# Kernel tuning notes

Hardware: AMD Instinct MI355X
Metric: run time of the kernel (lower is better)

The kernel has to match this reference:

```python
import jax, jax.numpy as jnp
import numpy as np

E = 8          # num_experts
TOP_K = 2
D = 1024       # hidden_size
I_MOE = 1024   # moe_intermediate_size (per-expert)
I_SH = 4096    # intermediate_size (shared expert)


def setup_inputs() -> dict:
    key = jax.random.key(0)
    ks = jax.random.split(key, 9)
    s = 0.02
    return {
        "hidden_states": jax.random.normal(ks[0], (2, 4096, D), dtype=jnp.float32),
        "gate_w": jax.random.normal(ks[1], (D, E), dtype=jnp.float32) * s,
        "eg": jax.random.normal(ks[2], (E, D, I_MOE), dtype=jnp.float32) * s,  # gate_proj per expert
        "eu": jax.random.normal(ks[3], (E, D, I_MOE), dtype=jnp.float32) * s,  # up_proj per expert
        "ed": jax.random.normal(ks[4], (E, I_MOE, D), dtype=jnp.float32) * s,  # down_proj per expert
        "sg": jax.random.normal(ks[5], (D, I_SH), dtype=jnp.float32) * s,
        "su": jax.random.normal(ks[6], (D, I_SH), dtype=jnp.float32) * s,
        "sd": jax.random.normal(ks[7], (I_SH, D), dtype=jnp.float32) * s,
        "shared_gate_w": jax.random.normal(ks[8], (D, 1), dtype=jnp.float32) * s,
    }


def _swiglu(x, wg, wu, wd):
    # down_proj(silu(gate_proj(x)) * up_proj(x))
    return (jax.nn.silu(x @ wg) * (x @ wu)) @ wd


def reference(hidden_states, gate_w, eg, eu, ed, sg, su, sd, shared_gate_w):
    B, S, Dm = hidden_states.shape
    x = hidden_states.reshape(-1, Dm)                     # [T, D]

    router_logits = x @ gate_w                            # [T, E]
    probs = jax.nn.softmax(router_logits.astype(jnp.float32), axis=-1)
    topw, topi = jax.lax.top_k(probs, TOP_K)              # [T, K]
    topw = topw / jnp.clip(jnp.sum(topw, axis=-1, keepdims=True), 1e-6)
    topw = topw.astype(x.dtype)

    # combine[t, e] = routing weight of expert e for token t (0 if unselected)
    combine = jnp.sum(jax.nn.one_hot(topi, E, dtype=x.dtype) * topw[..., None], axis=1)  # [T, E]

    out = jnp.zeros_like(x)
    for e in range(E):  # fixed small expert loop (structurally distinct weights)
        out = out + combine[:, e:e + 1] * _swiglu(x, eg[e], eu[e], ed[e])

    shared = _swiglu(x, sg, su, sd)
    shared_gate = jax.nn.sigmoid(x @ shared_gate_w)       # [T, 1]
    out = out + shared_gate * shared

    return out.reshape(B, S, Dm), router_logits
```

## Files before the change

### kernel.cpp

```cpp
#include <hip/hip_runtime.h>
#include <hip/hip_bf16.h>
#include <stdint.h>

#define T_TOK 8192
#define DDIM 1024
#define NEXP 8
#define IMOE 1024
#define ISH 4096
#define BK 64
#define PADTOT 17408

typedef __attribute__((ext_vector_type(8))) short short8;
typedef __attribute__((ext_vector_type(8))) __bf16 bf16x8;
typedef __attribute__((ext_vector_type(4))) float floatx4;

__device__ __forceinline__ unsigned short f2bf(float f) {
  union { float f; unsigned u; } v; v.f = f;
  unsigned r = v.u + 0x7fffu + ((v.u >> 16) & 1u);
  return (unsigned short)(r >> 16);
}

__device__ __forceinline__ floatx4 mfma16(short8 a, short8 b, floatx4 c) {
  return __builtin_amdgcn_mfma_f32_16x16x32_bf16(
      __builtin_bit_cast(bf16x8, a), __builtin_bit_cast(bf16x8, b), c, 0, 0, 0);
}

__device__ __forceinline__ void gload16(const void* g, void* l) {
  __builtin_amdgcn_global_load_lds((const __attribute__((address_space(1))) void*)g,
                                   (__attribute__((address_space(3))) void*)l, 16, 0, 0);
}



__global__ void k_cast(const float* __restrict__ src, unsigned short* __restrict__ dst, int n) {
  int i = (blockIdx.x * blockDim.x + threadIdx.x) * 4;
  if (i < n) {
    float4 v = *(const float4*)(src + i);
    ushort4 o;
    o.x = f2bf(v.x); o.y = f2bf(v.y); o.z = f2bf(v.z); o.w = f2bf(v.w);
    *(ushort4*)(dst + i) = o;
  }
}

__global__ void k_transpose_cast(const float* __restrict__ src, unsigned short* __restrict__ dst,
                                 int R, int C) {
  __shared__ float tile[32][33];
  int b = blockIdx.z;
  int c0 = blockIdx.x * 32, r0 = blockIdx.y * 32;
  const float* s = src + (size_t)b * R * C;
  unsigned short* d = dst + (size_t)b * R * C;
  int tx = threadIdx.x, ty = threadIdx.y;
#pragma unroll
  for (int j = 0; j < 32; j += 8)
    tile[ty + j][tx] = s[(size_t)(r0 + ty + j) * C + c0 + tx];
  __syncthreads();
#pragma unroll
  for (int j = 0; j < 32; j += 8)
    d[(size_t)(c0 + ty + j) * R + r0 + tx] = f2bf(tile[tx][ty + j]);
}


__global__ void k_router(const float* __restrict__ x, const float* __restrict__ gw,
                         const float* __restrict__ sgw, float* __restrict__ logits_out,
                         int* __restrict__ topi, float* __restrict__ topw,
                         float* __restrict__ sgate) {
  int wave = threadIdx.x >> 6;
  int lane = threadIdx.x & 63;
  int t = blockIdx.x * 4 + wave;
  const float* xr = x + (size_t)t * DDIM;
  float acc[9];
#pragma unroll
  for (int j = 0; j < 9; j++) acc[j] = 0.f;
  for (int d = lane; d < DDIM; d += 64) {
    float xv = xr[d];
    const float* g = gw + d * 8;
    float4 g0 = *(const float4*)g;
    float4 g1 = *(const float4*)(g + 4);
    acc[0] += xv * g0.x; acc[1] += xv * g0.y; acc[2] += xv * g0.z; acc[3] += xv * g0.w;
    acc[4] += xv * g1.x; acc[5] += xv * g1.y; acc[6] += xv * g1.z; acc[7] += xv * g1.w;
    acc[8] += xv * sgw[d];
  }
#pragma unroll
  for (int off = 32; off > 0; off >>= 1) {
#pragma unroll
    for (int j = 0; j < 9; j++) acc[j] += __shfl_xor(acc[j], off);
  }
  if (lane == 0) {
#pragma unroll
    for (int j = 0; j < 8; j++) logits_out[t * 8 + j] = acc[j];
    int i0 = 0;
#pragma unroll
    for (int j = 1; j < 8; j++) if (acc[j] > acc[i0]) i0 = j;
    int i1 = -1;
#pragma unroll
    for (int j = 0; j < 8; j++) {
      if (j == i0) continue;
      if (i1 < 0 || acc[j] > acc[i1]) i1 = j;
    }
    float e1 = expf(acc[i1] - acc[i0]);
    float inv = 1.f / (1.f + e1);
    topi[t * 2] = i0; topi[t * 2 + 1] = i1;
    topw[t * 2] = inv; topw[t * 2 + 1] = e1 * inv;
    sgate[t] = 1.f / (1.f + expf(-acc[8]));
  }
}

__global__ void k_hist(const int* __restrict__ topi, int* __restrict__ blockhist) {
  __shared__ int h[NEXP];
  if (threadIdx.x < NEXP) h[threadIdx.x] = 0;
  __syncthreads();
  int i = blockIdx.x * 256 + threadIdx.x;
  atomicAdd(&h[topi[i]], 1);
  __syncthreads();
  if (threadIdx.x < NEXP) blockhist[blockIdx.x * NEXP + threadIdx.x] = h[threadIdx.x];
}

__global__ void k_offsets(const int* __restrict__ blockhist, int* __restrict__ pseg,
                          int* __restrict__ rcnt, int* __restrict__ blockbase) {
  if (threadIdx.x == 0) {
    int tot[NEXP];
#pragma unroll
    for (int e = 0; e < NEXP; e++) tot[e] = 0;
    for (int b = 0; b < 64; b++)
      for (int e = 0; e < NEXP; e++) {
        blockbase[b * NEXP + e] = tot[e];
        tot[e] += blockhist[b * NEXP + e];
      }
    int s = 0;
    for (int e = 0; e < NEXP; e++) {
      rcnt[e] = tot[e];
      pseg[e] = s;
      s += (tot[e] + 127) & ~127;
    }
    pseg[NEXP] = s;
    for (int b = 0; b < 64; b++)
      for (int e = 0; e < NEXP; e++) blockbase[b * NEXP + e] += pseg[e];
  }
}

__global__ void k_scatter(const int* __restrict__ topi, const float* __restrict__ topw,
                          const int* __restrict__ blockbase,
                          int* __restrict__ ptok, float* __restrict__ pw) {
  __shared__ int cur[NEXP];
  if (threadIdx.x < NEXP) cur[threadIdx.x] = blockbase[blockIdx.x * NEXP + threadIdx.x];
  __syncthreads();
  int i = blockIdx.x * 256 + threadIdx.x;
  int e = topi[i];
  int pos = atomicAdd(&cur[e], 1);
  ptok[pos] = i >> 1;
  pw[pos] = topw[i];
}

__global__ void k_gather(const unsigned short* __restrict__ xb, const int* __restrict__ ptok,
                         unsigned short* __restrict__ xg) {
  int row = blockIdx.x * 2 + (threadIdx.x >> 7);
  int col = (threadIdx.x & 127) * 8;
  int tok = ptok[row];
  uint4 v = make_uint4(0, 0, 0, 0);
  if (tok >= 0 && tok < T_TOK) v = *(const uint4*)(xb + (size_t)tok * DDIM + col);
  *(uint4*)(xg + (size_t)row * DDIM + col) = v;
}

__global__ __launch_bounds__(256, 4) void k_gu_shared(
    const unsigned short* __restrict__ Xb,
    const unsigned short* __restrict__ BgT,
    const unsigned short* __restrict__ BuT,
    unsigned short* __restrict__ H)
{
  __shared__ __align__(16) unsigned short As[128 * BK];
  __shared__ __align__(16) unsigned short Bgs[64 * BK];
  __shared__ __align__(16) unsigned short Bus[64 * BK];

  const int tm0 = blockIdx.x * 128;
  const int tn0 = blockIdx.y * 64;
  const int tid = threadIdx.x;
  const int wave = tid >> 6, lane = tid & 63;
  const int wm = wave & 1, wn = wave >> 1;
  const int quad = lane >> 4, l16 = lane & 15;
  const int srow = lane >> 3;
  const int scol = ((lane & 7) ^ srow) * 8;

  floatx4 accg[4][2] = {};
  floatx4 accu[4][2] = {};

  for (int k0 = 0; k0 < DDIM; k0 += BK) {
#pragma unroll
    for (int s = 0; s < 4; s++) {
      int rb = (wave * 4 + s) * 8;
      gload16(Xb + (size_t)(tm0 + rb + srow) * DDIM + k0 + scol, As + rb * BK);
    }
#pragma unroll
    for (int s = 0; s < 2; s++) {
      int rb = (wave * 2 + s) * 8;
      gload16(BgT + (size_t)(tn0 + rb + srow) * DDIM + k0 + scol, Bgs + rb * BK);
      gload16(BuT + (size_t)(tn0 + rb + srow) * DDIM + k0 + scol, Bus + rb * BK);
    }
    __syncthreads();
#pragma unroll
    for (int ks = 0; ks < BK; ks += 32) {
      short8 af[4], bg[2], bu[2];
#pragma unroll
      for (int f = 0; f < 4; f++) {
        int r = wm * 64 + f * 16 + l16;
        af[f] = *(const short8*)(As + r * BK + ((((ks >> 3) + quad) ^ (r & 7)) << 3));
      }
#pragma unroll
      for (int f = 0; f < 2; f++) {
        int r = wn * 32 + f * 16 + l16;
        int off = r * BK + ((((ks >> 3) + quad) ^ (r & 7)) << 3);
        bg[f] = *(const short8*)(Bgs + off);
        bu[f] = *(const short8*)(Bus + off);
      }
#pragma unroll
      for (int fm = 0; fm < 4; fm++)
#pragma unroll
        for (int fn = 0; fn < 2; fn++) {
          accg[fm][fn] = mfma16(af[fm], bg[fn], accg[fm][fn]);
          accu[fm][fn] = mfma16(af[fm], bu[fn], accu[fm][fn]);
        }
    }
    __syncthreads();
  }
#pragma unroll
  for (int fm = 0; fm < 4; fm++)
#pragma unroll
    for (int reg = 0; reg < 4; reg++) {
      int r = tm0 + wm * 64 + fm * 16 + quad * 4 + reg;
#pragma unroll
      for (int fn = 0; fn < 2; fn++) {
        int c = tn0 + wn * 32 + fn * 16 + l16;
        float g = accg[fm][fn][reg];
        float u = accu[fm][fn][reg];
        float h = (g / (1.f + __expf(-g))) * u;
        H[(size_t)r * ISH + c] = f2bf(h);
      }
    }
}

__global__ __launch_bounds__(256, 4) void k_gu_expert(
    const unsigned short* __restrict__ Xg,
    const unsigned short* __restrict__ EgT,
    const unsigned short* __restrict__ EuT,
    const int* __restrict__ pseg,
    unsigned short* __restrict__ Hp)
{
  const int m0 = blockIdx.x * 128;
  if (m0 >= pseg[NEXP]) return;
  int e = 0;
#pragma unroll
  for (int j = 1; j < NEXP; j++) if (m0 >= pseg[j]) e = j;

  __shared__ __align__(16) unsigned short As[128 * BK];
  __shared__ __align__(16) unsigned short Bgs[64 * BK];
  __shared__ __align__(16) unsigned short Bus[64 * BK];

  const int tn0 = blockIdx.y * 64;
  const int tid = threadIdx.x;
  const int wave = tid >> 6, lane = tid & 63;
  const int wm = wave & 1, wn = wave >> 1;
  const int quad = lane >> 4, l16 = lane & 15;
  const int srow = lane >> 3;
  const int scol = ((lane & 7) ^ srow) * 8;

  const unsigned short* Bg = EgT + (size_t)e * IMOE * DDIM;
  const unsigned short* Bu = EuT + (size_t)e * IMOE * DDIM;

  floatx4 accg[4][2] = {};
  floatx4 accu[4][2] = {};

  for (int k0 = 0; k0 < DDIM; k0 += BK) {
#pragma unroll
    for (int s = 0; s < 4; s++) {
      int rb = (wave * 4 + s) * 8;
      gload16(Xg + (size_t)(m0 + rb + srow) * DDIM + k0 + scol, As + rb * BK);
    }
#pragma unroll
    for (int s = 0; s < 2; s++) {
      int rb = (wave * 2 + s) * 8;
      gload16(Bg + (size_t)(tn0 + rb + srow) * DDIM + k0 + scol, Bgs + rb * BK);
      gload16(Bu + (size_t)(tn0 + rb + srow) * DDIM + k0 + scol, Bus + rb * BK);
    }
    __syncthreads();
#pragma unroll
    for (int ks = 0; ks < BK; ks += 32) {
      short8 af[4], bg[2], bu[2];
#pragma unroll
      for (int f = 0; f < 4; f++) {
        int r = wm * 64 + f * 16 + l16;
        af[f] = *(const short8*)(As + r * BK + ((((ks >> 3) + quad) ^ (r & 7)) << 3));
      }
#pragma unroll
      for (int f = 0; f < 2; f++) {
        int r = wn * 32 + f * 16 + l16;
        int off = r * BK + ((((ks >> 3) + quad) ^ (r & 7)) << 3);
        bg[f] = *(const short8*)(Bgs + off);
        bu[f] = *(const short8*)(Bus + off);
      }
#pragma unroll
      for (int fm = 0; fm < 4; fm++)
#pragma unroll
        for (int fn = 0; fn < 2; fn++) {
          accg[fm][fn] = mfma16(af[fm], bg[fn], accg[fm][fn]);
          accu[fm][fn] = mfma16(af[fm], bu[fn], accu[fm][fn]);
        }
    }
    __syncthreads();
  }
#pragma unroll
  for (int fm = 0; fm < 4; fm++)
#pragma unroll
    for (int reg = 0; reg < 4; reg++) {
      int r = m0 + wm * 64 + fm * 16 + quad * 4 + reg;
#pragma unroll
      for (int fn = 0; fn < 2; fn++) {
        int c = tn0 + wn * 32 + fn * 16 + l16;
        float g = accg[fm][fn][reg];
        float u = accu[fm][fn][reg];
        Hp[(size_t)r * IMOE + c] = f2bf((g / (1.f + __expf(-g))) * u);
      }
    }
}

__global__ __launch_bounds__(256, 4) void k_down_shared(
    const unsigned short* __restrict__ Hsh,
    const unsigned short* __restrict__ SdT,
    const float* __restrict__ sgate,
    float* __restrict__ out)
{
  __shared__ __align__(16) unsigned short As[128 * BK];
  __shared__ __align__(16) unsigned short Bs[128 * BK];

  const int tm0 = blockIdx.x * 128;
  const int tn0 = blockIdx.y * 128;
  const int tid = threadIdx.x;
  const int wave = tid >> 6, lane = tid & 63;
  const int wm = wave & 1, wn = wave >> 1;
  const int quad = lane >> 4, l16 = lane & 15;
  const int srow = lane >> 3;
  const int scol = ((lane & 7) ^ srow) * 8;

  floatx4 acc[4][4] = {};

  for (int k0 = 0; k0 < ISH; k0 += BK) {
#pragma unroll
    for (int s = 0; s < 4; s++) {
      int rb = (wave * 4 + s) * 8;
      gload16(Hsh + (size_t)(tm0 + rb + srow) * ISH + k0 + scol, As + rb * BK);
      gload16(SdT + (size_t)(tn0 + rb + srow) * ISH + k0 + scol, Bs + rb * BK);
    }
    __syncthreads();
#pragma unroll
    for (int ks = 0; ks < BK; ks += 32) {
      short8 af[4], bfr[4];
#pragma unroll
      for (int f = 0; f < 4; f++) {
        int ra = wm * 64 + f * 16 + l16;
        int rb2 = wn * 64 + f * 16 + l16;
        af[f] = *(const short8*)(As + ra * BK + ((((ks >> 3) + quad) ^ (ra & 7)) << 3));
        bfr[f] = *(const short8*)(Bs + rb2 * BK + ((((ks >> 3) + quad) ^ (rb2 & 7)) << 3));
      }
#pragma unroll
      for (int fm = 0; fm < 4; fm++)
#pragma unroll
        for (int fn = 0; fn < 4; fn++)
          acc[fm][fn] = mfma16(af[fm], bfr[fn], acc[fm][fn]);
    }
    __syncthreads();
  }
#pragma unroll
  for (int fm = 0; fm < 4; fm++)
#pragma unroll
    for (int reg = 0; reg < 4; reg++) {
      int r = tm0 + wm * 64 + fm * 16 + quad * 4 + reg;
      float gt = sgate[r];
#pragma unroll
      for (int fn = 0; fn < 4; fn++) {
        int c = tn0 + wn * 64 + fn * 16 + l16;
        out[(size_t)r * DDIM + c] = gt * acc[fm][fn][reg];
      }
    }
}

__global__ __launch_bounds__(256, 4) void k_down_expert(
    const unsigned short* __restrict__ Hp,
    const unsigned short* __restrict__ EdT,
    const int* __restrict__ pseg,
    const int* __restrict__ rcnt,
    const int* __restrict__ ptok,
    const float* __restrict__ pw,
    float* __restrict__ out)
{
  const int m0 = blockIdx.x * 128;
  if (m0 >= pseg[NEXP]) return;
  int e = 0;
#pragma unroll
  for (int j = 1; j < NEXP; j++) if (m0 >= pseg[j]) e = j;
  const int sbase = pseg[e];
  const int cnt = rcnt[e];

  __shared__ __align__(16) unsigned short As[128 * BK];
  __shared__ __align__(16) unsigned short Bs[128 * BK];

  const int tn0 = blockIdx.y * 128;
  const int tid = threadIdx.x;
  const int wave = tid >> 6, lane = tid & 63;
  const int wm = wave & 1, wn = wave >> 1;
  const int quad = lane >> 4, l16 = lane & 15;
  const int srow = lane >> 3;
  const int scol = ((lane & 7) ^ srow) * 8;

  const unsigned short* B = EdT + (size_t)e * IMOE * DDIM;

  floatx4 acc[4][4] = {};

  for (int k0 = 0; k0 < IMOE; k0 += BK) {
#pragma unroll
    for (int s = 0; s < 4; s++) {
      int rb = (wave * 4 + s) * 8;
      gload16(Hp + (size_t)(m0 + rb + srow) * IMOE + k0 + scol, As + rb * BK);
      gload16(B + (size_t)(tn0 + rb + srow) * IMOE + k0 + scol, Bs + rb * BK);
    }
    __syncthreads();
#pragma unroll
    for (int ks = 0; ks < BK; ks += 32) {
      short8 af[4], bfr[4];
#pragma unroll
      for (int f = 0; f < 4; f++) {
        int ra = wm * 64 + f * 16 + l16;
        int rb2 = wn * 64 + f * 16 + l16;
        af[f] = *(const short8*)(As + ra * BK + ((((ks >> 3) + quad) ^ (ra & 7)) << 3));
        bfr[f] = *(const short8*)(Bs + rb2 * BK + ((((ks >> 3) + quad) ^ (rb2 & 7)) << 3));
      }
#pragma unroll
      for (int fm = 0; fm < 4; fm++)
#pragma unroll
        for (int fn = 0; fn < 4; fn++)
          acc[fm][fn] = mfma16(af[fm], bfr[fn], acc[fm][fn]);
    }
    __syncthreads();
  }
#pragma unroll
  for (int fm = 0; fm < 4; fm++)
#pragma unroll
    for (int reg = 0; reg < 4; reg++) {
      int grow = m0 + wm * 64 + fm * 16 + quad * 4 + reg;
      if (grow - sbase < cnt) {
        int t = ptok[grow];
        float w = pw[grow];
#pragma unroll
        for (int fn = 0; fn < 4; fn++) {
          int c = tn0 + wn * 64 + fn * 16 + l16;
          atomicAdd(&out[(size_t)t * DDIM + c], w * acc[fm][fn][reg]);
        }
      }
    }
}


extern "C" void kernel_launch(void* const* d_in, const int* in_sizes, int n_in,
                              void* d_out, int out_size, void* d_ws, size_t ws_size,
                              hipStream_t stream) {
  const float* x   = (const float*)d_in[0];
  const float* gw  = (const float*)d_in[1];
  const float* eg  = (const float*)d_in[2];
  const float* eu  = (const float*)d_in[3];
  const float* ed  = (const float*)d_in[4];
  const float* sg  = (const float*)d_in[5];
  const float* su  = (const float*)d_in[6];
  const float* sd  = (const float*)d_in[7];
  const float* sgw = (const float*)d_in[8];

  float* out    = (float*)d_out;
  float* logits = out + (size_t)T_TOK * DDIM;

  char* ws = (char*)d_ws;
  unsigned short* xb   = (unsigned short*)(ws + 0);
  unsigned short* egT  = (unsigned short*)(ws + 16777216);
  unsigned short* euT  = (unsigned short*)(ws + 33554432);
  unsigned short* edT  = (unsigned short*)(ws + 50331648);
  unsigned short* sgT  = (unsigned short*)(ws + 67108864);
  unsigned short* suT  = (unsigned short*)(ws + 75497472);
  unsigned short* sdT  = (unsigned short*)(ws + 83886080);
  unsigned short* hsh  = (unsigned short*)(ws + 92274688);
  unsigned short* xg   = (unsigned short*)(ws + 92274688);
  unsigned short* hp   = (unsigned short*)(ws + 159383552);
  int*   topi      = (int*)  (ws + 195035136);
  float* topw      = (float*)(ws + 195100672);
  float* sgate     = (float*)(ws + 195166208);
  int*   ptok      = (int*)  (ws + 195198976);
  float* pw        = (float*)(ws + 195268608);
  int*   blockhist = (int*)  (ws + 195338240);
  int*   blockbase = (int*)  (ws + 195340288);
  int*   pseg      = (int*)  (ws + 195342336);
  int*   rcnt      = (int*)  (ws + 195342400);

  k_cast<<<8192, 256, 0, stream>>>(x, xb, T_TOK * DDIM);
  k_transpose_cast<<<dim3(32, 32, 8), dim3(32, 8), 0, stream>>>(eg, egT, DDIM, IMOE);
  k_transpose_cast<<<dim3(32, 32, 8), dim3(32, 8), 0, stream>>>(eu, euT, DDIM, IMOE);
  k_transpose_cast<<<dim3(32, 32, 8), dim3(32, 8), 0, stream>>>(ed, edT, IMOE, DDIM);
  k_transpose_cast<<<dim3(128, 32, 1), dim3(32, 8), 0, stream>>>(sg, sgT, DDIM, ISH);
  k_transpose_cast<<<dim3(128, 32, 1), dim3(32, 8), 0, stream>>>(su, suT, DDIM, ISH);
  k_transpose_cast<<<dim3(32, 128, 1), dim3(32, 8), 0, stream>>>(sd, sdT, ISH, DDIM);

  k_router<<<T_TOK / 4, 256, 0, stream>>>(x, gw, sgw, logits, topi, topw, sgate);
  k_hist<<<64, 256, 0, stream>>>(topi, blockhist);
  k_offsets<<<1, 64, 0, stream>>>(blockhist, pseg, rcnt, blockbase);
  k_scatter<<<64, 256, 0, stream>>>(topi, topw, blockbase, ptok, pw);
  k_gather<<<PADTOT / 2, 256, 0, stream>>>(xb, ptok, xg);

  k_gu_expert<<<dim3(PADTOT / 128, 16), 256, 0, stream>>>(xg, egT, euT, pseg, hp);
  k_gu_shared<<<dim3(64, 64), 256, 0, stream>>>(xb, sgT, suT, hsh);
  k_down_shared<<<dim3(64, 8), 256, 0, stream>>>(hsh, sdT, sgate, out);
  k_down_expert<<<dim3(PADTOT / 128, 8), 256, 0, stream>>>(hp, edT, pseg, rcnt, ptok, pw, out);

  (void)in_sizes; (void)n_in; (void)out_size; (void)ws_size;
}
```

Before: 685.5 us.

## Replace gate/up GEMMs with 256x128 double-buffered 8-wave kernel with fused gather

Replaces the separate shared and expert gate/up GEMM kernels with one templated 512-thread kernel. It uses 256x128 tiles, double-buffered LDS, interleaved async loads with MFMA phases, and s_setprio scheduling hints. The expert path reads token rows straight from xb through ptok, which removes the separate gather kernel and its xg buffer. Expert segments are padded to 256 rows via a new vseg array. The cost is higher register and LDS pressure, and more wasted padding rows per expert.

Measured after the change: 680.4 us. No clear change (-0.8%).

```diff
diff --git a/kernel.cpp b/kernel.cpp
--- a/kernel.cpp
+++ b/kernel.cpp
@@ -116,7 +116,8 @@
 }
 
 __global__ void k_offsets(const int* __restrict__ blockhist, int* __restrict__ pseg,
-                          int* __restrict__ rcnt, int* __restrict__ blockbase) {
+                          int* __restrict__ rcnt, int* __restrict__ blockbase,
+                          int* __restrict__ vseg) {
   if (threadIdx.x == 0) {
     int tot[NEXP];
 #pragma unroll
@@ -126,13 +127,16 @@
         blockbase[b * NEXP + e] = tot[e];
         tot[e] += blockhist[b * NEXP + e];
       }
-    int s = 0;
+    int s = 0, vs = 0;
     for (int e = 0; e < NEXP; e++) {
       rcnt[e] = tot[e];
       pseg[e] = s;
+      vseg[e] = vs;
       s += (tot[e] + 127) & ~127;
+      vs += (tot[e] + 255) & ~255;
     }
     pseg[NEXP] = s;
+    vseg[NEXP] = vs;
     for (int b = 0; b < 64; b++)
       for (int e = 0; e < NEXP; e++) blockbase[b * NEXP + e] += pseg[e];
   }
@@ -151,175 +155,167 @@
   pw[pos] = topw[i];
 }
 
-__global__ void k_gather(const unsigned short* __restrict__ xb, const int* __restrict__ ptok,
-                         unsigned short* __restrict__ xg) {
-  int row = blockIdx.x * 2 + (threadIdx.x >> 7);
-  int col = (threadIdx.x & 127) * 8;
-  int tok = ptok[row];
-  uint4 v = make_uint4(0, 0, 0, 0);
-  if (tok >= 0 && tok < T_TOK) v = *(const uint4*)(xb + (size_t)tok * DDIM + col);
-  *(uint4*)(xg + (size_t)row * DDIM + col) = v;
-}
-
-__global__ __launch_bounds__(256, 4) void k_gu_shared(
-    const unsigned short* __restrict__ Xb,
-    const unsigned short* __restrict__ BgT,
-    const unsigned short* __restrict__ BuT,
+
+#define STG_A(NB, KK, P) gload16(ArowP[P] + (KK), &As[NB][((P)*64 + wave * 8) * BK])
+#define STG_G(NB, KK, P) gload16(Bgrow + (size_t)(P) * 64 * DDIM + (KK), &Bgs[NB][((P)*64 + wave * 8) * BK])
+#define STG_U(NB, KK, P) gload16(Burow + (size_t)(P) * 64 * DDIM + (KK), &Bus[NB][((P)*64 + wave * 8) * BK])
+
+#define GU_PHASE(CB, MGI, MGOFF, SW, G0, G1, U0, U1, ...)                     \
+  {                                                                           \
+    const unsigned short* Abp = &As[CB][ab + (MGOFF) * BK + (SW)];            \
+    short8 af0 = *(const short8*)(Abp);                                       \
+    short8 af1 = *(const short8*)(Abp + 16 * BK);                             \
+    short8 af2 = *(const short8*)(Abp + 32 * BK);                             \
+    short8 af3 = *(const short8*)(Abp + 48 * BK);                             \
+    __VA_ARGS__;                                                              \
+    __builtin_amdgcn_s_setprio(1);                                            \
+    accg[(MGI) + 0][0] = mfma16(af0, G0, accg[(MGI) + 0][0]);                 \
+    accu[(MGI) + 0][0] = mfma16(af0, U0, accu[(MGI) + 0][0]);                 \
+    accg[(MGI) + 0][1] = mfma16(af0, G1, accg[(MGI) + 0][1]);                 \
+    accu[(MGI) + 0][1] = mfma16(af0, U1, accu[(MGI) + 0][1]);                 \
+    accg[(MGI) + 1][0] = mfma16(af1, G0, accg[(MGI) + 1][0]);                 \
+    accu[(MGI) + 1][0] = mfma16(af1, U0, accu[(MGI) + 1][0]);                 \
+    accg[(MGI) + 1][1] = mfma16(af1, G1, accg[(MGI) + 1][1]);                 \
+    accu[(MGI) + 1][1] = mfma16(af1, U1, accu[(MGI) + 1][1]);                 \
+    accg[(MGI) + 2][0] = mfma16(af2, G0, accg[(MGI) + 2][0]);                 \
+    accu[(MGI) + 2][0] = mfma16(af2, U0, accu[(MGI) + 2][0]);                 \
+    accg[(MGI) + 2][1] = mfma16(af2, G1, accg[(MGI) + 2][1]);                 \
+    accu[(MGI) + 2][1] = mfma16(af2, U1, accu[(MGI) + 2][1]);                 \
+    accg[(MGI) + 3][0] = mfma16(af3, G0, accg[(MGI) + 3][0]);                 \
+    accu[(MGI) + 3][0] = mfma16(af3, U0, accu[(MGI) + 3][0]);                 \
+    accg[(MGI) + 3][1] = mfma16(af3, G1, accg[(MGI) + 3][1]);                 \
+    accu[(MGI) + 3][1] = mfma16(af3, U1, accu[(MGI) + 3][1]);                 \
+    __builtin_amdgcn_s_setprio(0);                                            \
+  }
+
+#define GU_TILE(CB, NB, KK)                                                         \
+  {                                                                                 \
+    const unsigned short* Bgb = &Bgs[CB][bb];                                       \
+    const unsigned short* Bub = &Bus[CB][bb];                                       \
+    short8 gA0 = *(const short8*)(Bgb + s0);                                        \
+    short8 gA1 = *(const short8*)(Bgb + 16 * BK + s0);                              \
+    short8 uA0 = *(const short8*)(Bub + s0);                                        \
+    short8 uA1 = *(const short8*)(Bub + 16 * BK + s0);                              \
+    GU_PHASE(CB, 0, 0, s0, gA0, gA1, uA0, uA1, STG_A(NB, KK, 0); STG_A(NB, KK, 2))  \
+    __builtin_amdgcn_s_barrier();                                                   \
+    short8 gB0 = *(const short8*)(Bgb + s1);                                        \
+    short8 gB1 = *(const short8*)(Bgb + 16 * BK + s1);                              \
+    short8 uB0 = *(const short8*)(Bub + s1);                                        \
+    short8 uB1 = *(const short8*)(Bub + 16 * BK + s1);                              \
+    GU_PHASE(CB, 0, 0, s1, gB0, gB1, uB0, uB1, STG_G(NB, KK, 0); STG_G(NB, KK, 1))  \
+    asm volatile("s_waitcnt vmcnt(4)" ::: "memory");                                \
+    __builtin_amdgcn_s_barrier();                                                   \
+    __builtin_amdgcn_sched_barrier(0);                                              \
+    GU_PHASE(CB, 4, 64, s0, gA0, gA1, uA0, uA1, STG_U(NB, KK, 0); STG_U(NB, KK, 1)) \
+    __builtin_amdgcn_s_barrier();                                                   \
+    GU_PHASE(CB, 4, 64, s1, gB0, gB1, uB0, uB1, STG_A(NB, KK, 1); STG_A(NB, KK, 3)) \
+    asm volatile("s_waitcnt vmcnt(2)" ::: "memory");                                \
+    __builtin_amdgcn_s_barrier();                                                   \
+    __builtin_amdgcn_sched_barrier(0);                                              \
+  }
+
+template <int LDC, bool EXPERT>
+__global__ __launch_bounds__(512) void k_gu8(
+    const unsigned short* __restrict__ Ag,
+    const unsigned short* __restrict__ Bg0,
+    const unsigned short* __restrict__ Bu0,
+    const int* __restrict__ pseg,
+    const int* __restrict__ vseg,
+    const int* __restrict__ ptok,
     unsigned short* __restrict__ H)
 {
-  __shared__ __align__(16) unsigned short As[128 * BK];
-  __shared__ __align__(16) unsigned short Bgs[64 * BK];
-  __shared__ __align__(16) unsigned short Bus[64 * BK];
-
-  const int tm0 = blockIdx.x * 128;
-  const int tn0 = blockIdx.y * 64;
+  const int m0 = blockIdx.x * 256;
+  const unsigned short* Bg = Bg0;
+  const unsigned short* Bu = Bu0;
+  int pbase = 0, plen = 0, voff0 = m0;
+  if constexpr (EXPERT) {
+    if (m0 >= vseg[NEXP]) return;
+    int e = 0;
+#pragma unroll
+    for (int j = 1; j < NEXP; j++) if (m0 >= vseg[j]) e = j;
+    Bg = Bg0 + (size_t)e * IMOE * DDIM;
+    Bu = Bu0 + (size_t)e * IMOE * DDIM;
+    pbase = pseg[e];
+    plen = pseg[e + 1] - pseg[e];
+    voff0 = m0 - vseg[e];
+  }
+  const int tn0 = blockIdx.y * 128;
+
+  __shared__ __align__(16) unsigned short As[2][256 * BK];
+  __shared__ __align__(16) unsigned short Bgs[2][128 * BK];
+  __shared__ __align__(16) unsigned short Bus[2][128 * BK];
+
   const int tid = threadIdx.x;
   const int wave = tid >> 6, lane = tid & 63;
-  const int wm = wave & 1, wn = wave >> 1;
+  const int wm = wave >> 2, wn = wave & 3;
   const int quad = lane >> 4, l16 = lane & 15;
   const int srow = lane >> 3;
   const int scol = ((lane & 7) ^ srow) * 8;
 
-  floatx4 accg[4][2] = {};
-  floatx4 accu[4][2] = {};
-
-  for (int k0 = 0; k0 < DDIM; k0 += BK) {
-#pragma unroll
-    for (int s = 0; s < 4; s++) {
-      int rb = (wave * 4 + s) * 8;
-      gload16(Xb + (size_t)(tm0 + rb + srow) * DDIM + k0 + scol, As + rb * BK);
-    }
-#pragma unroll
-    for (int s = 0; s < 2; s++) {
-      int rb = (wave * 2 + s) * 8;
-      gload16(BgT + (size_t)(tn0 + rb + srow) * DDIM + k0 + scol, Bgs + rb * BK);
-      gload16(BuT + (size_t)(tn0 + rb + srow) * DDIM + k0 + scol, Bus + rb * BK);
-    }
-    __syncthreads();
-#pragma unroll
-    for (int ks = 0; ks < BK; ks += 32) {
-      short8 af[4], bg[2], bu[2];
-#pragma unroll
-      for (int f = 0; f < 4; f++) {
-        int r = wm * 64 + f * 16 + l16;
-        af[f] = *(const short8*)(As + r * BK + ((((ks >> 3) + quad) ^ (r & 7)) << 3));
-      }
-#pragma unroll
-      for (int f = 0; f < 2; f++) {
-        int r = wn * 32 + f * 16 + l16;
-        int off = r * BK + ((((ks >> 3) + quad) ^ (r & 7)) << 3);
-        bg[f] = *(const short8*)(Bgs + off);
-        bu[f] = *(const short8*)(Bus + off);
-      }
-#pragma unroll
-      for (int fm = 0; fm < 4; fm++)
+  const unsigned short* ArowP[4];
+#pragma unroll
+  for (int P = 0; P < 4; P++) {
+    int vr = voff0 + P * 64 + wave * 8 + srow;
+    int row;
+    if constexpr (EXPERT) {
+      int tok = (vr < plen) ? ptok[pbase + vr] : 0;
+      if (tok < 0 || tok >= T_TOK) tok = 0;
+      row = tok;
+    } else {
+      row = vr;
+    }
+    ArowP[P] = Ag + (size_t)row * DDIM + scol;
+  }
+  const unsigned short* Bgrow = Bg + (size_t)(tn0 + wave * 8 + srow) * DDIM + scol;
+  const unsigned short* Burow = Bu + (size_t)(tn0 + wave * 8 + srow) * DDIM + scol;
+
+  const int ab = (wm * 128 + l16) * BK;
+  const int bb = (wn * 32 + l16) * BK;
+  const int s0 = ((quad) ^ (l16 & 7)) * 8;
+  const int s1 = ((quad + 4) ^ (l16 & 7)) * 8;
+
+  floatx4 accg[8][2] = {};
+  floatx4 accu[8][2] = {};
+
+  STG_A(0, 0, 0); STG_A(0, 0, 2);
+  STG_G(0, 0, 0); STG_G(0, 0, 1);
+  STG_U(0, 0, 0); STG_U(0, 0, 1);
+  STG_A(0, 0, 1); STG_A(0, 0, 3);
+  asm volatile("s_waitcnt vmcnt(2)" ::: "memory");
+  __builtin_amdgcn_s_barrier();
+  __builtin_amdgcn_sched_barrier(0);
+
+#pragma unroll 1
+  for (int k0 = 0; k0 < DDIM; k0 += 2 * BK) {
+    const int kA = k0 + BK;
+    const int kB = (k0 + 2 * BK < DDIM) ? (k0 + 2 * BK) : 0;
+    GU_TILE(0, 1, kA)
+    GU_TILE(1, 0, kB)
+  }
+
+#pragma unroll
+  for (int fm = 0; fm < 8; fm++)
+#pragma unroll
+    for (int reg = 0; reg < 4; reg++) {
+      int rr = voff0 + wm * 128 + fm * 16 + quad * 4 + reg;
+      bool ok = true;
+      int r = rr;
+      if constexpr (EXPERT) {
+        ok = rr < plen;
+        r = pbase + rr;
+      }
+      if (ok) {
 #pragma unroll
         for (int fn = 0; fn < 2; fn++) {
-          accg[fm][fn] = mfma16(af[fm], bg[fn], accg[fm][fn]);
-          accu[fm][fn] = mfma16(af[fm], bu[fn], accu[fm][fn]);
+          int c = tn0 + wn * 32 + fn * 16 + l16;
+          float g = accg[fm][fn][reg];
+          float u = accu[fm][fn][reg];
+          H[(size_t)r * LDC + c] = f2bf((g / (1.f + __expf(-g))) * u);
         }
-    }
-    __syncthreads();
-  }
-#pragma unroll
-  for (int fm = 0; fm < 4; fm++)
-#pragma unroll
-    for (int reg = 0; reg < 4; reg++) {
-      int r = tm0 + wm * 64 + fm * 16 + quad * 4 + reg;
-#pragma unroll
-      for (int fn = 0; fn < 2; fn++) {
-        int c = tn0 + wn * 32 + fn * 16 + l16;
-        float g = accg[fm][fn][reg];
-        float u = accu[fm][fn][reg];
-        float h = (g / (1.f + __expf(-g))) * u;
-        H[(size_t)r * ISH + c] = f2bf(h);
-      }
-    }
-}
-
-__global__ __launch_bounds__(256, 4) void k_gu_expert(
-    const unsigned short* __restrict__ Xg,
-    const unsigned short* __restrict__ EgT,
-    const unsigned short* __restrict__ EuT,
-    const int* __restrict__ pseg,
-    unsigned short* __restrict__ Hp)
-{
-  const int m0 = blockIdx.x * 128;
-  if (m0 >= pseg[NEXP]) return;
-  int e = 0;
-#pragma unroll
-  for (int j = 1; j < NEXP; j++) if (m0 >= pseg[j]) e = j;
-
-  __shared__ __align__(16) unsigned short As[128 * BK];
-  __shared__ __align__(16) unsigned short Bgs[64 * BK];
-  __shared__ __align__(16) unsigned short Bus[64 * BK];
-
-  const int tn0 = blockIdx.y * 64;
-  const int tid = threadIdx.x;
-  const int wave = tid >> 6, lane = tid & 63;
-  const int wm = wave & 1, wn = wave >> 1;
-  const int quad = lane >> 4, l16 = lane & 15;
-  const int srow = lane >> 3;
-  const int scol = ((lane & 7) ^ srow) * 8;
-
-  const unsigned short* Bg = EgT + (size_t)e * IMOE * DDIM;
-  const unsigned short* Bu = EuT + (size_t)e * IMOE * DDIM;
-
-  floatx4 accg[4][2] = {};
-  floatx4 accu[4][2] = {};
-
-  for (int k0 = 0; k0 < DDIM; k0 += BK) {
-#pragma unroll
-    for (int s = 0; s < 4; s++) {
-      int rb = (wave * 4 + s) * 8;
-      gload16(Xg + (size_t)(m0 + rb + srow) * DDIM + k0 + scol, As + rb * BK);
-    }
-#pragma unroll
-    for (int s = 0; s < 2; s++) {
-      int rb = (wave * 2 + s) * 8;
-      gload16(Bg + (size_t)(tn0 + rb + srow) * DDIM + k0 + scol, Bgs + rb * BK);
-      gload16(Bu + (size_t)(tn0 + rb + srow) * DDIM + k0 + scol, Bus + rb * BK);
-    }
-    __syncthreads();
-#pragma unroll
-    for (int ks = 0; ks < BK; ks += 32) {
-      short8 af[4], bg[2], bu[2];
-#pragma unroll
-      for (int f = 0; f < 4; f++) {
-        int r = wm * 64 + f * 16 + l16;
-        af[f] = *(const short8*)(As + r * BK + ((((ks >> 3) + quad) ^ (r & 7)) << 3));
-      }
-#pragma unroll
-      for (int f = 0; f < 2; f++) {
-        int r = wn * 32 + f * 16 + l16;
-        int off = r * BK + ((((ks >> 3) + quad) ^ (r & 7)) << 3);
-        bg[f] = *(const short8*)(Bgs + off);
-        bu[f] = *(const short8*)(Bus + off);
-      }
-#pragma unroll
-      for (int fm = 0; fm < 4; fm++)
-#pragma unroll
-        for (int fn = 0; fn < 2; fn++) {
-          accg[fm][fn] = mfma16(af[fm], bg[fn], accg[fm][fn]);
-          accu[fm][fn] = mfma16(af[fm], bu[fn], accu[fm][fn]);
-        }
-    }
-    __syncthreads();
-  }
-#pragma unroll
-  for (int fm = 0; fm < 4; fm++)
-#pragma unroll
-    for (int reg = 0; reg < 4; reg++) {
-      int r = m0 + wm * 64 + fm * 16 + quad * 4 + reg;
-#pragma unroll
-      for (int fn = 0; fn < 2; fn++) {
-        int c = tn0 + wn * 32 + fn * 16 + l16;
-        float g = accg[fm][fn][reg];
-        float u = accu[fm][fn][reg];
-        Hp[(size_t)r * IMOE + c] = f2bf((g / (1.f + __expf(-g))) * u);
-      }
-    }
-}
+      }
+    }
+}
+
 
 __global__ __launch_bounds__(256, 4) void k_down_shared(
     const unsigned short* __restrict__ Hsh,
@@ -482,7 +478,6 @@
   unsigned short* suT  = (unsigned short*)(ws + 75497472);
   unsigned short* sdT  = (unsigned short*)(ws + 83886080);
   unsigned short* hsh  = (unsigned short*)(ws + 92274688);
-  unsigned short* xg   = (unsigned short*)(ws + 92274688);
   unsigned short* hp   = (unsigned short*)(ws + 159383552);
   int*   topi      = (int*)  (ws + 195035136);
   float* topw      = (float*)(ws + 195100672);
@@ -493,6 +488,7 @@
   int*   blockbase = (int*)  (ws + 195340288);
   int*   pseg      = (int*)  (ws + 195342336);
   int*   rcnt      = (int*)  (ws + 195342400);
+  int*   vseg      = (int*)  (ws + 195342432);
 
   k_cast<<<8192, 256, 0, stream>>>(x, xb, T_TOK * DDIM);
   k_transpose_cast<<<dim3(32, 32, 8), dim3(32, 8), 0, stream>>>(eg, egT, DDIM, IMOE);
@@ -504,12 +500,11 @@
 
   k_router<<<T_TOK / 4, 256, 0, stream>>>(x, gw, sgw, logits, topi, topw, sgate);
   k_hist<<<64, 256, 0, stream>>>(topi, blockhist);
-  k_offsets<<<1, 64, 0, stream>>>(blockhist, pseg, rcnt, blockbase);
+  k_offsets<<<1, 64, 0, stream>>>(blockhist, pseg, rcnt, blockbase, vseg);
   k_scatter<<<64, 256, 0, stream>>>(topi, topw, blockbase, ptok, pw);
-  k_gather<<<PADTOT / 2, 256, 0, stream>>>(xb, ptok, xg);
-
-  k_gu_expert<<<dim3(PADTOT / 128, 16), 256, 0, stream>>>(xg, egT, euT, pseg, hp);
-  k_gu_shared<<<dim3(64, 64), 256, 0, stream>>>(xb, sgT, suT, hsh);
+
+  k_gu8<IMOE, true><<<dim3(72, IMOE / 128), 512, 0, stream>>>(xb, egT, euT, pseg, vseg, ptok, hp);
+  k_gu8<ISH, false><<<dim3(T_TOK / 256, ISH / 128), 512, 0, stream>>>(xb, sgT, suT, nullptr, nullptr, nullptr, hsh);
   k_down_shared<<<dim3(64, 8), 256, 0, stream>>>(hsh, sdT, sgate, out);
   k_down_expert<<<dim3(PADTOT / 128, 8), 256, 0, stream>>>(hp, edT, pseg, rcnt, ptok, pw, out);
 
```

## Fuse token gather into expert gate/up GEMM and add XCD-aware block swizzle

Applied to the files above, without the earlier changes.

Removes the separate gather kernel. The expert gate/up GEMM now reads activation rows straight from the bf16 input, using per-lane row pointers built from the permuted token index, so the padded gathered copy is never written or read back. Padding rows now load token 0 instead of zeros, which relies on the down kernel ignoring those rows. All four GEMMs switch to 1D launches with a block-ID remap that groups 8x8 output tiles per XCD, aiming for better L2 reuse of A and B tiles. The trade-off is indirect, less contiguous row loads in the fused GEMM.

After: 647.9 us. 5.5% less time.

```diff
diff --git a/kernel.cpp b/kernel.cpp
--- a/kernel.cpp
+++ b/kernel.cpp
@@ -28,6 +28,15 @@
 __device__ __forceinline__ void gload16(const void* g, void* l) {
   __builtin_amdgcn_global_load_lds((const __attribute__((address_space(1))) void*)g,
                                    (__attribute__((address_space(3))) void*)l, 16, 0, 0);
+}
+
+__device__ __forceinline__ void xcd_swz(int id, int gm, int gn, int& m, int& n) {
+  int cpx = (gm * gn) >> 3;
+  int wg = (id & 7) * cpx + (id >> 3);
+  int g = wg >> 6, r = wg & 63;
+  int gpr = gn >> 3;
+  m = ((g / gpr) << 3) | (r >> 3);
+  n = ((g % gpr) << 3) | (r & 7);
 }
 
 
@@ -151,28 +160,21 @@
   pw[pos] = topw[i];
 }
 
-__global__ void k_gather(const unsigned short* __restrict__ xb, const int* __restrict__ ptok,
-                         unsigned short* __restrict__ xg) {
-  int row = blockIdx.x * 2 + (threadIdx.x >> 7);
-  int col = (threadIdx.x & 127) * 8;
-  int tok = ptok[row];
-  uint4 v = make_uint4(0, 0, 0, 0);
-  if (tok >= 0 && tok < T_TOK) v = *(const uint4*)(xb + (size_t)tok * DDIM + col);
-  *(uint4*)(xg + (size_t)row * DDIM + col) = v;
-}
-
 __global__ __launch_bounds__(256, 4) void k_gu_shared(
     const unsigned short* __restrict__ Xb,
     const unsigned short* __restrict__ BgT,
     const unsigned short* __restrict__ BuT,
     unsigned short* __restrict__ H)
 {
+  int bm, bn;
+  xcd_swz(blockIdx.x, 64, 64, bm, bn);
+  const int tm0 = bm * 128;
+  const int tn0 = bn * 64;
+
   __shared__ __align__(16) unsigned short As[128 * BK];
   __shared__ __align__(16) unsigned short Bgs[64 * BK];
   __shared__ __align__(16) unsigned short Bus[64 * BK];
 
-  const int tm0 = blockIdx.x * 128;
-  const int tn0 = blockIdx.y * 64;
   const int tid = threadIdx.x;
   const int wave = tid >> 6, lane = tid & 63;
   const int wm = wave & 1, wn = wave >> 1;
@@ -238,13 +240,16 @@
 }
 
 __global__ __launch_bounds__(256, 4) void k_gu_expert(
-    const unsigned short* __restrict__ Xg,
+    const unsigned short* __restrict__ Xb,
     const unsigned short* __restrict__ EgT,
     const unsigned short* __restrict__ EuT,
     const int* __restrict__ pseg,
+    const int* __restrict__ ptok,
     unsigned short* __restrict__ Hp)
 {
-  const int m0 = blockIdx.x * 128;
+  int bm, bn;
+  xcd_swz(blockIdx.x, PADTOT / 128, 16, bm, bn);
+  const int m0 = bm * 128;
   if (m0 >= pseg[NEXP]) return;
   int e = 0;
 #pragma unroll
@@ -254,7 +259,7 @@
   __shared__ __align__(16) unsigned short Bgs[64 * BK];
   __shared__ __align__(16) unsigned short Bus[64 * BK];
 
-  const int tn0 = blockIdx.y * 64;
+  const int tn0 = bn * 64;
   const int tid = threadIdx.x;
   const int wave = tid >> 6, lane = tid & 63;
   const int wm = wave & 1, wn = wave >> 1;
@@ -265,6 +270,14 @@
   const unsigned short* Bg = EgT + (size_t)e * IMOE * DDIM;
   const unsigned short* Bu = EuT + (size_t)e * IMOE * DDIM;
 
+  const unsigned short* ArowP[4];
+#pragma unroll
+  for (int s = 0; s < 4; s++) {
+    int tok = ptok[m0 + (wave * 4 + s) * 8 + srow];
+    if (tok < 0 || tok >= T_TOK) tok = 0;
+    ArowP[s] = Xb + (size_t)tok * DDIM + scol;
+  }
+
   floatx4 accg[4][2] = {};
   floatx4 accu[4][2] = {};
 
@@ -272,7 +285,7 @@
 #pragma unroll
     for (int s = 0; s < 4; s++) {
       int rb = (wave * 4 + s) * 8;
-      gload16(Xg + (size_t)(m0 + rb + srow) * DDIM + k0 + scol, As + rb * BK);
+      gload16(ArowP[s] + k0, As + rb * BK);
     }
 #pragma unroll
     for (int s = 0; s < 2; s++) {
@@ -330,8 +343,10 @@
   __shared__ __align__(16) unsigned short As[128 * BK];
   __shared__ __align__(16) unsigned short Bs[128 * BK];
 
-  const int tm0 = blockIdx.x * 128;
-  const int tn0 = blockIdx.y * 128;
+  int bm, bn;
+  xcd_swz(blockIdx.x, 64, 8, bm, bn);
+  const int tm0 = bm * 128;
+  const int tn0 = bn * 128;
   const int tid = threadIdx.x;
   const int wave = tid >> 6, lane = tid & 63;
   const int wm = wave & 1, wn = wave >> 1;
@@ -390,7 +405,9 @@
     const float* __restrict__ pw,
     float* __restrict__ out)
 {
-  const int m0 = blockIdx.x * 128;
+  int bm, bn;
+  xcd_swz(blockIdx.x, PADTOT / 128, 8, bm, bn);
+  const int m0 = bm * 128;
   if (m0 >= pseg[NEXP]) return;
   int e = 0;
 #pragma unroll
@@ -401,7 +418,7 @@
   __shared__ __align__(16) unsigned short As[128 * BK];
   __shared__ __align__(16) unsigned short Bs[128 * BK];
 
-  const int tn0 = blockIdx.y * 128;
+  const int tn0 = bn * 128;
   const int tid = threadIdx.x;
   const int wave = tid >> 6, lane = tid & 63;
   const int wm = wave & 1, wn = wave >> 1;
@@ -482,7 +499,6 @@
   unsigned short* suT  = (unsigned short*)(ws + 75497472);
   unsigned short* sdT  = (unsigned short*)(ws + 83886080);
   unsigned short* hsh  = (unsigned short*)(ws + 92274688);
-  unsigned short* xg   = (unsigned short*)(ws + 92274688);
   unsigned short* hp   = (unsigned short*)(ws + 159383552);
   int*   topi      = (int*)  (ws + 195035136);
   float* topw      = (float*)(ws + 195100672);
@@ -506,12 +522,11 @@
   k_hist<<<64, 256, 0, stream>>>(topi, blockhist);
   k_offsets<<<1, 64, 0, stream>>>(blockhist, pseg, rcnt, blockbase);
   k_scatter<<<64, 256, 0, stream>>>(topi, topw, blockbase, ptok, pw);
-  k_gather<<<PADTOT / 2, 256, 0, stream>>>(xb, ptok, xg);
-
-  k_gu_expert<<<dim3(PADTOT / 128, 16), 256, 0, stream>>>(xg, egT, euT, pseg, hp);
-  k_gu_shared<<<dim3(64, 64), 256, 0, stream>>>(xb, sgT, suT, hsh);
-  k_down_shared<<<dim3(64, 8), 256, 0, stream>>>(hsh, sdT, sgate, out);
-  k_down_expert<<<dim3(PADTOT / 128, 8), 256, 0, stream>>>(hp, edT, pseg, rcnt, ptok, pw, out);
+
+  k_gu_expert<<<(PADTOT / 128) * 16, 256, 0, stream>>>(xb, egT, euT, pseg, ptok, hp);
+  k_gu_shared<<<64 * 64, 256, 0, stream>>>(xb, sgT, suT, hsh);
+  k_down_shared<<<64 * 8, 256, 0, stream>>>(hsh, sdT, sgate, out);
+  k_down_expert<<<(PADTOT / 128) * 8, 256, 0, stream>>>(hp, edT, pseg, rcnt, ptok, pw, out);
 
   (void)in_sizes; (void)n_in; (void)out_size; (void)ws_size;
 }
```
